# Kernel tuning notes

Hardware: AMD Instinct MI355X
Metric: run time of the kernel (lower is better)

Reference implementation:

```python
import jax, jax.numpy as jnp
import numpy as np

LN_EPS = 1e-5

def _layer_norm(x, g, b):
    m = jnp.mean(x, axis=-1, keepdims=True)
    v = jnp.mean((x - m) ** 2, axis=-1, keepdims=True)
    return (x - m) / jnp.sqrt(v + LN_EPS) * g + b

def setup_inputs() -> dict:
    key = jax.random.key(0)
    ks = jax.random.split(key, 16)
    B, L, D = 4, 2048, 1024
    DF = 4 * D
    s_in = 1.0 / np.sqrt(D)
    s_ff = 1.0 / np.sqrt(DF)
    # torch init of phazor: exp(2j*pi*arange(D)/D) * |randn|
    ang = 2.0 * np.pi * jnp.arange(D, dtype=jnp.float32) / D
    mag = jnp.abs(jax.random.normal(ks[0], (D,), jnp.float32))
    return {
        "x": jax.random.normal(ks[1], (B, L, D), jnp.float32),
        "hidden_real": jax.random.normal(ks[2], (B, D), jnp.float32),
        "hidden_imag": jax.random.normal(ks[3], (B, D), jnp.float32),
        "phazor_real": mag * jnp.cos(ang),
        "phazor_imag": mag * jnp.sin(ang),
        "phazor_init_real": jax.random.normal(ks[4], (D,), jnp.float32),
        "phazor_init_imag": jax.random.normal(ks[5], (D,), jnp.float32),
        "ln_gamma": jnp.ones((D,), jnp.float32),
        "ln_beta": jnp.zeros((D,), jnp.float32),
        "fc_w": jax.random.uniform(ks[6], (D, D), jnp.float32, -s_in, s_in),
        "fc_b": jax.random.uniform(ks[7], (D,), jnp.float32, -s_in, s_in),
        "w1": jax.random.uniform(ks[8], (DF, D), jnp.float32, -s_in, s_in),
        "b1": jax.random.uniform(ks[9], (DF,), jnp.float32, -s_in, s_in),
        "w2": jax.random.uniform(ks[10], (D, DF), jnp.float32, -s_ff, s_ff),
        "b2": jax.random.uniform(ks[11], (D,), jnp.float32, -s_ff, s_ff),
    }

def _spiral_conv(x, hidden, phazor_p, phazor_init):
    # x: [B,L,D] real, hidden: [B,D] complex
    B, L, D = x.shape
    amag = jnp.abs(phazor_p)
    phazor = phazor_p / amag * jnp.exp(-amag)                      # [D]
    prog = jnp.power(phazor[None, :], jnp.arange(L)[:, None])      # [L,D]
    filt = prog * phazor_init[None, :]                             # [L,D]
    filt_fft = jnp.fft.fft(filt, n=2 * L, axis=0)                  # [2L,D]
    x_fft = jnp.fft.fft(x.astype(jnp.complex64), n=2 * L, axis=1)  # [B,2L,D]
    conv = jnp.fft.ifft(filt_fft[None] * x_fft, axis=1)[:, :L]     # [B,L,D]
    conv_with_past = conv + jax.lax.stop_gradient(hidden)[:, None, :] * prog[None] * phazor[None, None]
    return conv_with_past.real, conv_with_past

def reference(x, hidden_real, hidden_imag, phazor_real, phazor_imag,
              phazor_init_real, phazor_init_imag, ln_gamma, ln_beta,
              fc_w, fc_b, w1, b1, w2, b2):
    hidden = hidden_real + 1j * hidden_imag
    phazor_p = phazor_real + 1j * phazor_imag
    phazor_init = phazor_init_real + 1j * phazor_init_imag

    x_res = x
    xn = _layer_norm(x, ln_gamma, ln_beta)
    s, new_hidden = _spiral_conv(xn, hidden, phazor_p, phazor_init)
    y = jax.nn.silu(jnp.einsum('bld,ed->ble', x, fc_w) + fc_b)
    h = s * y + x_res                      # dropout is identity (p=0 / eval)
    hn = _layer_norm(h, ln_gamma, ln_beta) # same LayerNorm instance reused
    ffn = jnp.einsum('blf,df->bld', jax.nn.silu(jnp.einsum('bld,fd->blf', hn, w1) + b1), w2) + b2
    out = ffn + h
    return out, new_hidden
```

## Files before the change

kernel.cpp:

```cpp
#include <hip/hip_runtime.h>

typedef unsigned short u16;
typedef unsigned int u32;
typedef float f32x4 __attribute__((ext_vector_type(4)));
typedef __bf16 bf16x8 __attribute__((ext_vector_type(8)));
typedef unsigned short u16x4 __attribute__((ext_vector_type(4)));

__device__ __forceinline__ float b2f(u16 u) {
    return __uint_as_float(((u32)u) << 16);
}
__device__ __forceinline__ u16 f2b(float f) {
    u32 u = __float_as_uint(f);
    return (u16)((u + 0x7FFFu + ((u >> 16) & 1u)) >> 16);
}
__device__ __forceinline__ bool is_f32(const u32* flag) {
    return flag[0] == 0x3F800000u;
}
__device__ __forceinline__ float lda(const void* p, size_t i, bool f) {
    return f ? ((const float*)p)[i] : b2f(((const u16*)p)[i]);
}
__device__ __forceinline__ void cmul(float& xr, float& xi, float yr, float yi) {
    float tr = xr * yr - xi * yi;
    xi = xr * yi + xi * yr;
    xr = tr;
}
__device__ __forceinline__ void gl2lds16(const void* g, void* l) {
    __builtin_amdgcn_global_load_lds(
        (const __attribute__((address_space(1))) void*)g,
        (__attribute__((address_space(3))) void*)l, 16, 0, 0);
}
__device__ __forceinline__ void wg_barrier() {
    asm volatile("" ::: "memory");
    __builtin_amdgcn_sched_barrier(0);
    __builtin_amdgcn_s_barrier();
    __builtin_amdgcn_sched_barrier(0);
    asm volatile("" ::: "memory");
}
#define VWAIT0 { asm volatile("s_waitcnt vmcnt(0)" ::: "memory"); __builtin_amdgcn_sched_barrier(0); }
#define VWAIT2 { asm volatile("s_waitcnt vmcnt(2)" ::: "memory"); __builtin_amdgcn_sched_barrier(0); }
#define VWAIT4 { asm volatile("s_waitcnt vmcnt(4)" ::: "memory"); __builtin_amdgcn_sched_barrier(0); }
#define LGKM0  { asm volatile("s_waitcnt lgkmcnt(0)" ::: "memory"); __builtin_amdgcn_sched_barrier(0); }

struct CvtArgs {
    const void* src[9];
    u16* dst[9];
    int n2[9];
    int tot;
};
__global__ __launch_bounds__(256) void cvtm_k(CvtArgs a, const u32* __restrict__ flag) {
    bool f = is_f32(flag);
    int i = blockIdx.x * 256 + threadIdx.x;
    if (i >= a.tot) return;
    int s = 0, base = 0;
    while (i - base >= a.n2[s]) { base += a.n2[s]; s++; }
    int k = i - base;
    if (f) {
        float2 v = ((const float2*)a.src[s])[k];
        ((u32*)a.dst[s])[k] = (u32)f2b(v.x) | ((u32)f2b(v.y) << 16);
    } else {
        ((u32*)a.dst[s])[k] = ((const u32*)a.src[s])[k];
    }
}

__global__ __launch_bounds__(256) void ln_k(const u16* __restrict__ x,
                                            const u16* __restrict__ g,
                                            const u16* __restrict__ be,
                                            u16* __restrict__ o, int D) {
    int row = blockIdx.x;
    const u16* xr = x + (size_t)row * D;
    int tid = threadIdx.x;
    float s = 0.f, s2 = 0.f;
    for (int i = tid * 4; i < D; i += 1024) {
        u16x4 v = *(const u16x4*)&xr[i];
        float a0 = b2f(v.x), a1 = b2f(v.y), a2 = b2f(v.z), a3 = b2f(v.w);
        s  += (a0 + a1) + (a2 + a3);
        s2 += (a0 * a0 + a1 * a1) + (a2 * a2 + a3 * a3);
    }
    for (int off = 32; off > 0; off >>= 1) {
        s  += __shfl_down(s,  off, 64);
        s2 += __shfl_down(s2, off, 64);
    }
    __shared__ float red[8];
    int wave = tid >> 6;
    if ((tid & 63) == 0) { red[wave * 2] = s; red[wave * 2 + 1] = s2; }
    __syncthreads();
    if (tid == 0) {
        float ts = 0.f, ts2 = 0.f;
        for (int w = 0; w < 4; w++) { ts += red[w * 2]; ts2 += red[w * 2 + 1]; }
        float m = ts / D;
        float v = ts2 / D - m * m;
        red[0] = m;
        red[1] = rsqrtf(v + 1e-5f);
    }
    __syncthreads();
    float m = red[0], inv = red[1];
    u16* orow = o + (size_t)row * D;
    for (int i = tid * 4; i < D; i += 1024) {
        u16x4 v = *(const u16x4*)&xr[i];
        u16x4 gv = *(const u16x4*)&g[i];
        u16x4 bv = *(const u16x4*)&be[i];
        u16x4 r;
        r.x = f2b((b2f(v.x) - m) * inv * b2f(gv.x) + b2f(bv.x));
        r.y = f2b((b2f(v.y) - m) * inv * b2f(gv.y) + b2f(bv.y));
        r.z = f2b((b2f(v.z) - m) * inv * b2f(gv.z) + b2f(bv.z));
        r.w = f2b((b2f(v.w) - m) * inv * b2f(gv.w) + b2f(bv.w));
        *(u16x4*)&orow[i] = r;
    }
}

__global__ __launch_bounds__(256) void scan_partial_k(const u16* __restrict__ xn,
                                                      const void* __restrict__ phr_,
                                                      const void* __restrict__ phi_,
                                                      float2* __restrict__ T,
                                                      int L, int D, int C, int Kc,
                                                      const u32* __restrict__ flag) {
    bool f = is_f32(flag);
    int tid = blockIdx.x * 256 + threadIdx.x;
    int d = tid % D;
    int c = (tid / D) % C;
    int b = tid / (D * C);
    float pr = lda(phr_, d, f), pi = lda(phi_, d, f);
    float amag = fmaxf(sqrtf(pr * pr + pi * pi), 1e-12f);
    float sc = __expf(-amag) / amag;
    float phr = pr * sc, phi = pi * sc;
    float Tr = 0.f, Ti = 0.f;
    const u16* xp = xn + ((size_t)b * L + (size_t)c * Kc) * D + d;
    for (int t = 0; t < Kc; t++) {
        float x = b2f(xp[(size_t)t * D]);
        float nr = phr * Tr - phi * Ti + x;
        Ti = phr * Ti + phi * Tr;
        Tr = nr;
    }
    T[tid] = make_float2(Tr, Ti);
}

__global__ __launch_bounds__(256) void scan_prefix_k(const void* __restrict__ phr_,
                                                     const void* __restrict__ phi_,
                                                     const float2* __restrict__ T,
                                                     float2* __restrict__ E,
                                                     int D, int C, int Kc,
                                                     const u32* __restrict__ flag) {
    bool f = is_f32(flag);
    int tid = blockIdx.x * 256 + threadIdx.x;
    int d = tid % D;
    int b = tid / D;
    float pr = lda(phr_, d, f), pi = lda(phi_, d, f);
    float amag = fmaxf(sqrtf(pr * pr + pi * pi), 1e-12f);
    float sc = __expf(-amag) / amag;
    float phr = pr * sc, phi = pi * sc;
    float kr = phr, ki = phi;
    for (int s = 1; s < Kc; s <<= 1) cmul(kr, ki, kr, ki);
    float cr = 0.f, ci = 0.f;
    for (int c = 0; c < C; c++) {
        size_t i = ((size_t)b * C + c) * D + d;
        E[i] = make_float2(cr, ci);
        float2 t = T[i];
        cmul(cr, ci, kr, ki);
        cr += t.x; ci += t.y;
    }
}

__global__ __launch_bounds__(256) void scan_final_k(const u16* __restrict__ xn,
                                                    const void* __restrict__ phr_,
                                                    const void* __restrict__ phi_,
                                                    const void* __restrict__ pir_,
                                                    const void* __restrict__ pii_,
                                                    const void* __restrict__ hr_,
                                                    const void* __restrict__ hi_,
                                                    const float2* __restrict__ E,
                                                    u16* __restrict__ sws,
                                                    void* __restrict__ dout,
                                                    int MD, int out_elems,
                                                    int L, int D, int C, int Kc,
                                                    const u32* __restrict__ flag) {
    bool f = is_f32(flag);
    int tid = blockIdx.x * 256 + threadIdx.x;
    int d = tid % D;
    int c = (tid / D) % C;
    int b = tid / (D * C);
    float pr = lda(phr_, d, f), pi = lda(phi_, d, f);
    float amag = fmaxf(sqrtf(pr * pr + pi * pi), 1e-12f);
    float sc = __expf(-amag) / amag;
    float phr = pr * sc, phi = pi * sc;
    float kr = phr, ki = phi;
    for (int s = 1; s < Kc; s <<= 1) cmul(kr, ki, kr, ki);
    float Pr = phr, Pi = phi;
    for (int j = 0; j < c; j++) cmul(Pr, Pi, kr, ki);
    float ir = lda(pir_, d, f), ii = lda(pii_, d, f);
    float hr = lda(hr_, (size_t)b * D + d, f), hi = lda(hi_, (size_t)b * D + d, f);
    float2 e = E[tid];
    float Sr = e.x, Si = e.y;
    const bool full = (out_elems >= 3 * MD);
    size_t mbase = (size_t)b * L + (size_t)c * Kc;
    for (int t = 0; t < Kc; t++) {
        size_t off = (mbase + t) * D + d;
        float x = b2f(xn[off]);
        float nr = phr * Sr - phi * Si + x;
        Si = phr * Si + phi * Sr;
        Sr = nr;
        float cr = ir * Sr - ii * Si + hr * Pr - hi * Pi;
        float ci = ir * Si + ii * Sr + hr * Pi + hi * Pr;
        sws[off] = f2b(cr);
        if (f) {
            float* fo = (float*)dout;
            if (full) {
                *(float2*)&fo[(size_t)MD + 2 * off] = make_float2(cr, ci);
            } else {
                fo[(size_t)MD + off] = cr;
            }
        } else {
            u16* uo = (u16*)dout;
            if (full) {
                *(u32*)&uo[(size_t)MD + 2 * off] =
                    (u32)f2b(cr) | ((u32)f2b(ci) << 16);
            } else {
                uo[(size_t)MD + off] = f2b(cr);
            }
        }
        cmul(Pr, Pi, phr, phi);
    }
}

template <int MODE>
__global__ __launch_bounds__(256) void gemm128(const u16* __restrict__ A,
                                               const u16* __restrict__ Bm,
                                               int M, int N, int K,
                                               const u16* __restrict__ bias,
                                               const u16* __restrict__ sbuf,
                                               const u16* __restrict__ xbuf,
                                               u16* __restrict__ out,
                                               void* __restrict__ outv,
                                               const u32* __restrict__ flag) {
    __shared__ u16 As[2][128 * 64];
    __shared__ u16 Bs[2][128 * 64];
    const int tid = threadIdx.x;
    const int wave = tid >> 6, lane = tid & 63;
    const int quad = lane >> 4, l16 = lane & 15;

    const int NT = N >> 7;
    const int j = blockIdx.x;
    const int gsize = 8 * NT;
    const int mg  = j / gsize;
    const int rem = j - mg * gsize;
    const int nt  = rem >> 3;
    const int mi  = rem & 7;
    const int bm = (mg * 8 + mi) * 128, bn = nt * 128;

    const int wrow = (wave >> 1) * 64, wcol = (wave & 1) * 64;

    f32x4 acc[4][4] = {};

    const int lr = lane >> 3;
    const int sl = (lane & 7) ^ lr;
    const size_t goff = (size_t)lr * K + sl * 8;
    const size_t K8 = (size_t)K * 8;
    const u16* aG = A  + (size_t)(bm + wave * 32) * K + goff;
    const u16* bG = Bm + (size_t)(bn + wave * 32) * K + goff;

#define STG8(B_, t_) { \
        const u16* ga = aG + (size_t)(t_) * 64; \
        const u16* gb = bG + (size_t)(t_) * 64; \
        gl2lds16(ga,          &As[B_][(wave * 32) * 64]); \
        gl2lds16(ga + K8,     &As[B_][(wave * 32 + 8) * 64]); \
        gl2lds16(ga + 2 * K8, &As[B_][(wave * 32 + 16) * 64]); \
        gl2lds16(ga + 3 * K8, &As[B_][(wave * 32 + 24) * 64]); \
        gl2lds16(gb,          &Bs[B_][(wave * 32) * 64]); \
        gl2lds16(gb + K8,     &Bs[B_][(wave * 32 + 8) * 64]); \
        gl2lds16(gb + 2 * K8, &Bs[B_][(wave * 32 + 16) * 64]); \
        gl2lds16(gb + 3 * K8, &Bs[B_][(wave * 32 + 24) * 64]); }

#define RD_A(B_, m_, ks_) (*(const bf16x8*)&As[B_][(wrow + (m_) * 16 + l16) * 64 + \
        ((((ks_) * 4 + quad) ^ (l16 & 7)) << 3)])
#define RD_B(B_, n_, ks_) (*(const bf16x8*)&Bs[B_][(wcol + (n_) * 16 + l16) * 64 + \
        ((((ks_) * 4 + quad) ^ (l16 & 7)) << 3)])

#define FMK(mm, nn, ks) acc[mm][nn] = __builtin_amdgcn_mfma_f32_16x16x32_bf16( \
        av[mm][ks], bv[nn][ks], acc[mm][ks == 0 ? nn : nn], 0, 0, 0)
#undef FMK
#define FMK(mm, nn, ks) acc[mm][nn] = __builtin_amdgcn_mfma_f32_16x16x32_bf16( \
        av[mm][ks], bv[nn][ks], acc[mm][nn], 0, 0, 0)

#define ITER128(CUR, t_) { \
        const bool stg = (t_) + 1 < KT; \
        if (stg) STG8(CUR ^ 1, (t_) + 1); \
        av[0][0] = RD_A(CUR, 0, 0); av[1][0] = RD_A(CUR, 1, 0); \
        av[2][0] = RD_A(CUR, 2, 0); av[3][0] = RD_A(CUR, 3, 0); \
        bv[0][0] = RD_B(CUR, 0, 0); bv[1][0] = RD_B(CUR, 1, 0); \
        bv[2][0] = RD_B(CUR, 2, 0); bv[3][0] = RD_B(CUR, 3, 0); \
        av[0][1] = RD_A(CUR, 0, 1); av[1][1] = RD_A(CUR, 1, 1); \
        av[2][1] = RD_A(CUR, 2, 1); av[3][1] = RD_A(CUR, 3, 1); \
        bv[0][1] = RD_B(CUR, 0, 1); bv[1][1] = RD_B(CUR, 1, 1); \
        bv[2][1] = RD_B(CUR, 2, 1); bv[3][1] = RD_B(CUR, 3, 1); \
        FMK(0, 0, 0); FMK(0, 1, 0); FMK(1, 0, 0); FMK(1, 1, 0); \
        FMK(0, 2, 0); FMK(0, 3, 0); FMK(1, 2, 0); FMK(1, 3, 0); \
        FMK(2, 0, 0); FMK(2, 1, 0); FMK(3, 0, 0); FMK(3, 1, 0); \
        FMK(2, 2, 0); FMK(2, 3, 0); FMK(3, 2, 0); FMK(3, 3, 0); \
        FMK(0, 0, 1); FMK(0, 1, 1); FMK(1, 0, 1); FMK(1, 1, 1); \
        FMK(0, 2, 1); FMK(0, 3, 1); FMK(1, 2, 1); FMK(1, 3, 1); \
        FMK(2, 0, 1); FMK(2, 1, 1); FMK(3, 0, 1); FMK(3, 1, 1); \
        FMK(2, 2, 1); FMK(2, 3, 1); FMK(3, 2, 1); FMK(3, 3, 1); \
        if (stg) { VWAIT0 } \
        wg_barrier(); }

    bf16x8 av[4][2], bv[4][2];
    const int KT = K >> 6;

    STG8(0, 0);
    VWAIT0; wg_barrier();

    for (int t = 0; t < KT; t += 2) {
        ITER128(0, t);
        ITER128(1, t + 1);
    }

    bool f = (MODE == 2) ? is_f32(flag) : false;
#pragma unroll
    for (int m = 0; m < 4; m++) {
#pragma unroll
        for (int n = 0; n < 4; n++) {
            int colg = bn + wcol + n * 16 + l16;
            float bsv = b2f(bias[colg]);
#pragma unroll
            for (int r = 0; r < 4; r++) {
                int rowg = bm + wrow + m * 16 + quad * 4 + r;
                size_t idx = (size_t)rowg * N + colg;
                float v = acc[m][n][r] + bsv;
                if (MODE == 0) {
                    float y = v / (1.f + __expf(-v));
                    float hv = b2f(sbuf[idx]) * y + b2f(xbuf[idx]);
                    out[idx] = f2b(hv);
                } else if (MODE == 1) {
                    float y = v / (1.f + __expf(-v));
                    out[idx] = f2b(y);
                } else {
                    float o = v + b2f(xbuf[idx]);
                    if (f) ((float*)outv)[idx] = o;
                    else   ((u16*)outv)[idx] = f2b(o);
                }
            }
        }
    }
#undef STG8
#undef RD_A
#undef RD_B
#undef FMK
#undef ITER128
}

template <int MODE, int BN>
__global__ __launch_bounds__(512) void gemm_nt(const u16* __restrict__ A,
                                               const u16* __restrict__ Bm,
                                               int M, int N, int K,
                                               const u16* __restrict__ bias,
                                               const u16* __restrict__ sbuf,
                                               const u16* __restrict__ xbuf,
                                               u16* __restrict__ out,
                                               void* __restrict__ outv,
                                               const u32* __restrict__ flag) {
    __shared__ u16 As[2][256 * 64];
    __shared__ u16 Bs[2][BN * 64];
    const int tid = threadIdx.x;
    const int wave = tid >> 6, lane = tid & 63;
    const int quad = lane >> 4, l16 = lane & 15;

    const int NT = N / BN;
    const int j = blockIdx.x;
    const int gsize = 8 * NT;
    const int mg  = j / gsize;
    const int rem = j - mg * gsize;
    const int nt  = rem >> 3;
    const int mi  = rem & 7;
    const int bm = (mg * 8 + mi) * 256, bn = nt * BN;

    const int wrow = (wave >> 2) * 128, wcol = (wave & 3) * 64;

    f32x4 acc[8][4] = {};

    const int lr = lane >> 3;
    const int sl = (lane & 7) ^ lr;
    const size_t goff = (size_t)lr * K + sl * 8;
    const size_t K8 = (size_t)K * 8;
    const u16* aG = A  + (size_t)(bm + wave * 16) * K + goff;
    const u16* bG = Bm + (size_t)(bn + wave * 16) * K + goff;

#define STG_A(B_, t_, h_) { \
        const u16* ga = aG + (size_t)(t_) * 64 + (size_t)(h_) * 128 * K; \
        gl2lds16(ga,      &As[B_][((h_) * 128 + wave * 16) * 64]); \
        gl2lds16(ga + K8, &As[B_][((h_) * 128 + wave * 16 + 8) * 64]); }
#define STG_B(B_, t_, h_) { \
        const u16* gb = bG + (size_t)(t_) * 64 + (size_t)(h_) * 128 * K; \
        gl2lds16(gb,      &Bs[B_][((h_) * 128 + wave * 16) * 64]); \
        gl2lds16(gb + K8, &Bs[B_][((h_) * 128 + wave * 16 + 8) * 64]); }

#define RDA(B_, m_, ks_) (*(const bf16x8*)&As[B_][(wrow + (m_) * 16 + l16) * 64 + \
        ((((ks_) * 4 + quad) ^ (l16 & 7)) << 3)])
#define RDB(B_, n_, ks_) (*(const bf16x8*)&Bs[B_][(wcol + (n_) * 16 + l16) * 64 + \
        ((((ks_) * 4 + quad) ^ (l16 & 7)) << 3)])

#define LDA4(RB, mh) { \
        av[0][0] = RDA(RB, (mh) * 4 + 0, 0); av[0][1] = RDA(RB, (mh) * 4 + 0, 1); \
        av[1][0] = RDA(RB, (mh) * 4 + 1, 0); av[1][1] = RDA(RB, (mh) * 4 + 1, 1); \
        av[2][0] = RDA(RB, (mh) * 4 + 2, 0); av[2][1] = RDA(RB, (mh) * 4 + 2, 1); \
        av[3][0] = RDA(RB, (mh) * 4 + 3, 0); av[3][1] = RDA(RB, (mh) * 4 + 3, 1); }
#define LDB2(RB, nh) { \
        bv[(nh) * 2 + 0][0] = RDB(RB, (nh) * 2 + 0, 0); \
        bv[(nh) * 2 + 0][1] = RDB(RB, (nh) * 2 + 0, 1); \
        bv[(nh) * 2 + 1][0] = RDB(RB, (nh) * 2 + 1, 0); \
        bv[(nh) * 2 + 1][1] = RDB(RB, (nh) * 2 + 1, 1); }

#define FM(mi_, ni_, ks_) acc[mi_][ni_] = __builtin_amdgcn_mfma_f32_16x16x32_bf16( \
        av[(mi_) & 3][ks_], bv[ni_][ks_], acc[mi_][ni_], 0, 0, 0)
#define MFMA16(mh, nh) { \
        __builtin_amdgcn_s_setprio(1); \
        FM((mh)*4+0, (nh)*2+0, 0); FM((mh)*4+0, (nh)*2+1, 0); \
        FM((mh)*4+1, (nh)*2+0, 0); FM((mh)*4+1, (nh)*2+1, 0); \
        FM((mh)*4+2, (nh)*2+0, 0); FM((mh)*4+2, (nh)*2+1, 0); \
        FM((mh)*4+3, (nh)*2+0, 0); FM((mh)*4+3, (nh)*2+1, 0); \
        FM((mh)*4+0, (nh)*2+0, 1); FM((mh)*4+0, (nh)*2+1, 1); \
        FM((mh)*4+1, (nh)*2+0, 1); FM((mh)*4+1, (nh)*2+1, 1); \
        FM((mh)*4+2, (nh)*2+0, 1); FM((mh)*4+2, (nh)*2+1, 1); \
        FM((mh)*4+3, (nh)*2+0, 1); FM((mh)*4+3, (nh)*2+1, 1); \
        __builtin_amdgcn_s_setprio(0); }

    bf16x8 av[4][2], bv[4][2];
    const int KT = K >> 6;

    STG_A(0, 0, 0); STG_B(0, 0, 0); STG_B(0, 0, 1); STG_A(0, 0, 1);
    VWAIT4; wg_barrier();
#define TILE256(RB, SB, t_) { \
        const bool stg = (t_) + 1 < KT; \
         \
        LDA4(RB, 0); LDB2(RB, 0); \
        if (stg) STG_A(SB, (t_) + 1, 0);       \
        wg_barrier(); LGKM0; \
        MFMA16(0, 0); \
        if (stg) { VWAIT4 } else { VWAIT2 }    \
        wg_barrier(); \
         \
        LDB2(RB, 1); \
        if (stg) STG_B(SB, (t_) + 1, 0);       \
        wg_barrier(); LGKM0; \
        MFMA16(0, 1); \
        if (stg) { VWAIT4 } else { VWAIT0 }    \
        wg_barrier(); \
         \
        LDA4(RB, 1); \
        if (stg) STG_B(SB, (t_) + 1, 1);       \
        wg_barrier(); LGKM0; \
        MFMA16(1, 0); \
        wg_barrier(); \
         \
        if (stg) STG_A(SB, (t_) + 1, 1);       \
        wg_barrier(); LGKM0; \
        MFMA16(1, 1); \
        if (stg) { VWAIT4 }                    \
        wg_barrier(); }
    for (int t = 0; t < KT; t += 2) {
        TILE256(0, 1, t);
        TILE256(1, 0, t + 1);
    }
#undef TILE256

    bool f = (MODE == 2) ? is_f32(flag) : false;
#pragma unroll
    for (int m = 0; m < 8; m++) {
#pragma unroll
        for (int n = 0; n < 4; n++) {
            int colg = bn + wcol + n * 16 + l16;
            float bsv = b2f(bias[colg]);
#pragma unroll
            for (int r = 0; r < 4; r++) {
                int rowg = bm + wrow + m * 16 + quad * 4 + r;
                size_t idx = (size_t)rowg * N + colg;
                float v = acc[m][n][r] + bsv;
                if (MODE == 0) {
                    float y = v / (1.f + __expf(-v));
                    float hv = b2f(sbuf[idx]) * y + b2f(xbuf[idx]);
                    out[idx] = f2b(hv);
                } else if (MODE == 1) {
                    float y = v / (1.f + __expf(-v));
                    out[idx] = f2b(y);
                } else {
                    float o = v + b2f(xbuf[idx]);
                    if (f) ((float*)outv)[idx] = o;
                    else   ((u16*)outv)[idx] = f2b(o);
                }
            }
        }
    }
#undef STG_A
#undef STG_B
#undef RDA
#undef RDB
#undef LDA4
#undef LDB2
#undef FM
#undef MFMA16
}

extern "C" void kernel_launch(void* const* d_in, const int* in_sizes, int n_in,
                              void* d_out, int out_size, void* d_ws, size_t ws_size,
                              hipStream_t stream) {
    const void* x   = d_in[0];
    const void* hr  = d_in[1];
    const void* hi  = d_in[2];
    const void* phr = d_in[3];
    const void* phi = d_in[4];
    const void* pir = d_in[5];
    const void* pii = d_in[6];
    const void* g   = d_in[7];
    const void* be  = d_in[8];
    const void* fcw = d_in[9];
    const void* fcb = d_in[10];
    const void* w1  = d_in[11];
    const void* b1  = d_in[12];
    const void* w2  = d_in[13];
    const void* b2  = d_in[14];
    const u32* flag = (const u32*)g;

    const int D  = in_sizes[3];
    const int Bb = in_sizes[1] / D;
    const int L  = in_sizes[0] / (Bb * D);
    const int DF = in_sizes[12];
    const int M  = Bb * L;
    const int Kc = 32, C = L / Kc;
    const int MD = M * D;

    char* ws = (char*)d_ws;
    size_t MD2 = (size_t)MD * 2;
    u16*    xb  = (u16*)(ws);
    u16*    xn  = (u16*)(ws + MD2);
    u16*    sws = (u16*)(ws + 2 * MD2);
    float2* T   = (float2*)(ws + 3 * MD2);
    float2* E   = (float2*)(ws + 3 * MD2 + (size_t)Bb * C * D * 8);
    u16*    a1  = (u16*)(ws);
    u16*    h   = (u16*)(ws + 4 * MD2);
    u16*    hn  = (u16*)(ws + 5 * MD2);
    char*   wp  = ws + 6 * MD2;
    u16* fcwb = (u16*)wp; wp += (size_t)D * D * 2;
    u16* w1b  = (u16*)wp; wp += (size_t)DF * D * 2;
    u16* w2b  = (u16*)wp; wp += (size_t)D * DF * 2;
    u16* fcbb = (u16*)wp; wp += (size_t)D * 2;
    u16* b1b  = (u16*)wp; wp += (size_t)DF * 2;
    u16* b2b  = (u16*)wp; wp += (size_t)D * 2;
    u16* gb   = (u16*)wp; wp += (size_t)D * 2;
    u16* bb   = (u16*)wp; wp += (size_t)D * 2;

    CvtArgs ca;
    const void* srcs[9] = { x, fcw, w1, w2, fcb, b1, b2, g, be };
    u16* dsts[9] = { xb, fcwb, w1b, w2b, fcbb, b1b, b2b, gb, bb };
    size_t ns[9] = { (size_t)MD, (size_t)D * D, (size_t)DF * D, (size_t)D * DF,
                     (size_t)D, (size_t)DF, (size_t)D, (size_t)D, (size_t)D };
    int tot = 0;
    for (int i = 0; i < 9; i++) {
        ca.src[i] = srcs[i];
        ca.dst[i] = dsts[i];
        ca.n2[i] = (int)(ns[i] / 2);
        tot += ca.n2[i];
    }
    ca.tot = tot;
    cvtm_k<<<(tot + 255) / 256, 256, 0, stream>>>(ca, flag);

    ln_k<<<M, 256, 0, stream>>>(xb, gb, bb, xn, D);
    scan_partial_k<<<(Bb * C * D) / 256, 256, 0, stream>>>(xn, phr, phi, T, L, D, C, Kc, flag);
    scan_prefix_k<<<(Bb * D) / 256, 256, 0, stream>>>(phr, phi, T, E, D, C, Kc, flag);
    scan_final_k<<<(Bb * C * D) / 256, 256, 0, stream>>>(xn, phr, phi, pir, pii, hr, hi,
                                                         E, sws, d_out, MD, out_size,
                                                         L, D, C, Kc, flag);
    gemm128<0><<<(M / 128) * (D / 128), 256, 0, stream>>>(xb, fcwb, M, D, D, fcbb, sws, xb, h, nullptr, flag);
    ln_k<<<M, 256, 0, stream>>>(h, gb, bb, hn, D);
    gemm_nt<1, 256><<<(M / 256) * (DF / 256), 512, 0, stream>>>(hn, w1b, M, DF, D, b1b, nullptr, nullptr, a1, nullptr, flag);
    gemm128<2><<<(M / 128) * (D / 128), 256, 0, stream>>>(a1, w2b, M, D, DF, b2b, nullptr, h, nullptr, d_out, flag);
}
```

Baseline: 412.6 us.

## Replace direct global-to-LDS loads with register-staged two-deep prefetch in GEMM

The GEMM main loop no longer uses direct global-to-LDS copies. It now loads K-tiles into registers two iterations ahead and writes them to the other LDS buffer one iteration ahead, so global latency is hidden by a deeper software pipeline. The cost is extra VGPRs for two register sets, explicit ds_write traffic, and an LGKM wait in place of the vmcnt wait, which may reduce occupancy or add LDS store pressure.

```diff
diff --git a/kernel.cpp b/kernel.cpp
--- a/kernel.cpp
+++ b/kernel.cpp
@@ -257,17 +257,28 @@
     const u16* aG = A  + (size_t)(bm + wave * 32) * K + goff;
     const u16* bG = Bm + (size_t)(bn + wave * 32) * K + goff;
 
-#define STG8(B_, t_) { \
+    f32x4 ra[2][4], rb[2][4];
+
+#define GLD(SET, t_) { \
         const u16* ga = aG + (size_t)(t_) * 64; \
         const u16* gb = bG + (size_t)(t_) * 64; \
-        gl2lds16(ga,          &As[B_][(wave * 32) * 64]); \
-        gl2lds16(ga + K8,     &As[B_][(wave * 32 + 8) * 64]); \
-        gl2lds16(ga + 2 * K8, &As[B_][(wave * 32 + 16) * 64]); \
-        gl2lds16(ga + 3 * K8, &As[B_][(wave * 32 + 24) * 64]); \
-        gl2lds16(gb,          &Bs[B_][(wave * 32) * 64]); \
-        gl2lds16(gb + K8,     &Bs[B_][(wave * 32 + 8) * 64]); \
-        gl2lds16(gb + 2 * K8, &Bs[B_][(wave * 32 + 16) * 64]); \
-        gl2lds16(gb + 3 * K8, &Bs[B_][(wave * 32 + 24) * 64]); }
+        ra[SET][0] = *(const f32x4*)ga; \
+        ra[SET][1] = *(const f32x4*)(ga + K8); \
+        ra[SET][2] = *(const f32x4*)(ga + 2 * K8); \
+        ra[SET][3] = *(const f32x4*)(ga + 3 * K8); \
+        rb[SET][0] = *(const f32x4*)gb; \
+        rb[SET][1] = *(const f32x4*)(gb + K8); \
+        rb[SET][2] = *(const f32x4*)(gb + 2 * K8); \
+        rb[SET][3] = *(const f32x4*)(gb + 3 * K8); }
+#define DSW(SET, B_) { \
+        *(f32x4*)&As[B_][(wave * 32 +  0) * 64 + lane * 8] = ra[SET][0]; \
+        *(f32x4*)&As[B_][(wave * 32 +  8) * 64 + lane * 8] = ra[SET][1]; \
+        *(f32x4*)&As[B_][(wave * 32 + 16) * 64 + lane * 8] = ra[SET][2]; \
+        *(f32x4*)&As[B_][(wave * 32 + 24) * 64 + lane * 8] = ra[SET][3]; \
+        *(f32x4*)&Bs[B_][(wave * 32 +  0) * 64 + lane * 8] = rb[SET][0]; \
+        *(f32x4*)&Bs[B_][(wave * 32 +  8) * 64 + lane * 8] = rb[SET][1]; \
+        *(f32x4*)&Bs[B_][(wave * 32 + 16) * 64 + lane * 8] = rb[SET][2]; \
+        *(f32x4*)&Bs[B_][(wave * 32 + 24) * 64 + lane * 8] = rb[SET][3]; }
 
 #define RD_A(B_, m_, ks_) (*(const bf16x8*)&As[B_][(wrow + (m_) * 16 + l16) * 64 + \
         ((((ks_) * 4 + quad) ^ (l16 & 7)) << 3)])
@@ -275,14 +286,11 @@
         ((((ks_) * 4 + quad) ^ (l16 & 7)) << 3)])
 
 #define FMK(mm, nn, ks) acc[mm][nn] = __builtin_amdgcn_mfma_f32_16x16x32_bf16( \
-        av[mm][ks], bv[nn][ks], acc[mm][ks == 0 ? nn : nn], 0, 0, 0)
-#undef FMK
-#define FMK(mm, nn, ks) acc[mm][nn] = __builtin_amdgcn_mfma_f32_16x16x32_bf16( \
         av[mm][ks], bv[nn][ks], acc[mm][nn], 0, 0, 0)
 
 #define ITER128(CUR, t_) { \
-        const bool stg = (t_) + 1 < KT; \
-        if (stg) STG8(CUR ^ 1, (t_) + 1); \
+        if ((t_) + 2 < KT) GLD(CUR, (t_) + 2); \
+        if ((t_) + 1 < KT) DSW(CUR ^ 1, CUR ^ 1); \
         av[0][0] = RD_A(CUR, 0, 0); av[1][0] = RD_A(CUR, 1, 0); \
         av[2][0] = RD_A(CUR, 2, 0); av[3][0] = RD_A(CUR, 3, 0); \
         bv[0][0] = RD_B(CUR, 0, 0); bv[1][0] = RD_B(CUR, 1, 0); \
@@ -299,14 +307,16 @@
         FMK(0, 2, 1); FMK(0, 3, 1); FMK(1, 2, 1); FMK(1, 3, 1); \
         FMK(2, 0, 1); FMK(2, 1, 1); FMK(3, 0, 1); FMK(3, 1, 1); \
         FMK(2, 2, 1); FMK(2, 3, 1); FMK(3, 2, 1); FMK(3, 3, 1); \
-        if (stg) { VWAIT0 } \
+        LGKM0; \
         wg_barrier(); }
 
     bf16x8 av[4][2], bv[4][2];
     const int KT = K >> 6;
 
-    STG8(0, 0);
-    VWAIT0; wg_barrier();
+    GLD(0, 0);
+    GLD(1, 1);
+    DSW(0, 0);
+    LGKM0; wg_barrier();
 
     for (int t = 0; t < KT; t += 2) {
         ITER128(0, t);
@@ -340,7 +350,8 @@
             }
         }
     }
-#undef STG8
+#undef GLD
+#undef DSW
 #undef RD_A
 #undef RD_B
 #undef FMK
```

Result: no change. 416.3 us (+0.9%).
